# Kernel optimization log

Hardware: AMD Instinct MI355X
Metric: run time of the kernel (lower is better)

Reference implementation:

```python
import jax, jax.numpy as jnp
import numpy as np
import math

V, C, H, L, S, K = 1024, 768, 12, 8, 1024, 10
B, T = 8, 1024
D = C // H


def setup_inputs():
    key = jax.random.key(0)
    ks = jax.random.split(key, 16)
    std = 0.02
    def nrm(k, shape):
        return jax.random.normal(k, shape, jnp.float32) * std
    return {
        "idx": jax.random.randint(ks[0], (B, T), 0, V),
        "y": jax.random.randint(ks[1], (B,), 0, K),
        "tok_emb": nrm(ks[2], (V, C)),
        "pos_emb": nrm(ks[3], (1, S, C)),
        "class_emb": nrm(ks[4], (K, C)),
        "ln1_w": jnp.ones((L, C)), "ln1_b": jnp.zeros((L, C)),
        "attn_w": nrm(ks[5], (L, C, 3 * C)), "attn_b": jnp.zeros((L, 3 * C)),
        "proj_w": nrm(ks[6], (L, C, C)), "proj_b": jnp.zeros((L, C)),
        "ln2_w": jnp.ones((L, C)), "ln2_b": jnp.zeros((L, C)),
        "mlp_w1": nrm(ks[7], (L, C, 4 * C)), "mlp_b1": jnp.zeros((L, 4 * C)),
        "mlp_w2": nrm(ks[8], (L, 4 * C, C)), "mlp_b2": jnp.zeros((L, C)),
        "ln_f_w": jnp.ones((C,)), "ln_f_b": jnp.zeros((C,)),
        "head_w": nrm(ks[9], (C, V)),
    }


def _ln(x, w, b, eps=1e-5):
    m = jnp.mean(x, -1, keepdims=True)
    v = jnp.mean((x - m) ** 2, -1, keepdims=True)
    return (x - m) * jax.lax.rsqrt(v + eps) * w + b


def reference(idx, y, tok_emb, pos_emb, class_emb, ln1_w, ln1_b, attn_w, attn_b,
              proj_w, proj_b, ln2_w, ln2_b, mlp_w1, mlp_b1, mlp_w2, mlp_b2,
              ln_f_w, ln_f_b, head_w):
    Bb, Tt = idx.shape
    # token + positional + class-conditioning embeddings (dropout in eval mode)
    x = tok_emb[idx] + pos_emb[:, :Tt, :] + class_emb[y][:, None, :]
    mask = jnp.tril(jnp.ones((Tt, Tt), bool))
    scale = 1.0 / math.sqrt(D)

    def block(x, p):
        l1w, l1b, aw, ab, pw, pb, l2w, l2b, w1, b1, w2, b2 = p
        h = _ln(x, l1w, l1b)
        qkv = h @ aw + ab                      # [B,T,3C]
        q, k, v = jnp.split(qkv, 3, axis=-1)
        q = q.reshape(Bb, Tt, H, D).transpose(0, 2, 1, 3)
        k = k.reshape(Bb, Tt, H, D).transpose(0, 2, 1, 3)
        v = v.reshape(Bb, Tt, H, D).transpose(0, 2, 1, 3)
        att = jnp.einsum('bhqd,bhkd->bhqk', q, k) * scale
        att = jnp.where(mask, att, -jnp.inf)
        att = jax.nn.softmax(att, axis=-1)
        o = jnp.einsum('bhqk,bhkd->bhqd', att, v)
        o = o.transpose(0, 2, 1, 3).reshape(Bb, Tt, C)
        x = x + o @ pw + pb
        h2 = _ln(x, l2w, l2b)
        x = x + jax.nn.gelu(h2 @ w1 + b1, approximate=False) @ w2 + b2
        return x, None

    x, _ = jax.lax.scan(block, x, (ln1_w, ln1_b, attn_w, attn_b, proj_w, proj_b,
                                   ln2_w, ln2_b, mlp_w1, mlp_b1, mlp_w2, mlp_b2))
    return _ln(x, ln_f_w, ln_f_b) @ head_w
```

## Files before the change

### kernel.cpp

```cpp
#include <hip/hip_runtime.h>
#include <math.h>

#define V_  1024
#define C_  768
#define H_  12
#define L_  8
#define B_  8
#define T_  1024
#define M_  (B_ * T_)
#define C3_ (3 * C_)
#define C4_ (4 * C_)

#define SCL2E 0.18033688011112042592f

typedef __bf16 bf16;
typedef __bf16 bf16x8 __attribute__((ext_vector_type(8)));
typedef float  f32x4  __attribute__((ext_vector_type(4)));
typedef unsigned int u32x4 __attribute__((ext_vector_type(4)));

#define GLDS16(g, l) __builtin_amdgcn_global_load_lds(                       \
    (const __attribute__((address_space(1))) void*)(g),                      \
    (__attribute__((address_space(3))) void*)(l), 16, 0, 0)

__device__ __forceinline__ unsigned short bfb(float f) {
    bf16 h = (bf16)f;
    return __builtin_bit_cast(unsigned short, h);
}

__global__ __launch_bounds__(256) void embed_kernel(
    const int* __restrict__ idx, const int* __restrict__ y,
    const float* __restrict__ tok, const float* __restrict__ pos,
    const float* __restrict__ cls, float* __restrict__ x) {
    int row = blockIdx.x;
    int b = row >> 10, t = row & (T_ - 1);
    int tid = threadIdx.x;
    const float* tr = tok + (size_t)idx[row] * C_;
    const float* pr = pos + (size_t)t * C_;
    const float* cr = cls + (size_t)y[b] * C_;
    float* xr = x + (size_t)row * C_;
    for (int c = tid; c < C_; c += 256)
        xr[c] = tr[c] + pr[c] + cr[c];
}

__device__ __forceinline__ float block_sum256(float v, float* red) {
#pragma unroll
    for (int off = 32; off > 0; off >>= 1) v += __shfl_down(v, off);
    __syncthreads();
    if ((threadIdx.x & 63) == 0) red[threadIdx.x >> 6] = v;
    __syncthreads();
    return red[0] + red[1] + red[2] + red[3];
}

__global__ __launch_bounds__(256) void ln_kernel(
    const float* __restrict__ in, const float* __restrict__ w,
    const float* __restrict__ b, bf16* __restrict__ out) {
    __shared__ float red[4];
    int row = blockIdx.x, tid = threadIdx.x;
    const float* xr = in + (size_t)row * C_;
    float v0 = xr[tid], v1 = xr[tid + 256], v2 = xr[tid + 512];
    float s = block_sum256(v0 + v1 + v2, red);
    float m = s * (1.0f / C_);
    float d0 = v0 - m, d1 = v1 - m, d2 = v2 - m;
    float s2 = block_sum256(d0 * d0 + d1 * d1 + d2 * d2, red);
    float rs = rsqrtf(s2 * (1.0f / C_) + 1e-5f);
    bf16* orow = out + (size_t)row * C_;
    orow[tid]       = (bf16)(d0 * rs * w[tid]       + b[tid]);
    orow[tid + 256] = (bf16)(d1 * rs * w[tid + 256] + b[tid + 256]);
    orow[tid + 512] = (bf16)(d2 * rs * w[tid + 512] + b[tid + 512]);
}

__global__ __launch_bounds__(256) void wt_kernel(
    const float* __restrict__ W, bf16* __restrict__ Wt, int K, int N) {
    __shared__ float ts[32][33];
    const size_t sz = (size_t)K * N;
    const float* Ws = W + blockIdx.z * sz;
    bf16* Wts = Wt + blockIdx.z * sz;
    int n0 = blockIdx.x * 32, k0 = blockIdx.y * 32;
    int tx = threadIdx.x & 31, ty = threadIdx.x >> 5;
#pragma unroll
    for (int i = 0; i < 4; ++i)
        ts[ty + i * 8][tx] = Ws[(size_t)(k0 + ty + i * 8) * N + n0 + tx];
    __syncthreads();
#pragma unroll
    for (int i = 0; i < 4; ++i)
        Wts[(size_t)(n0 + ty + i * 8) * K + k0 + tx] = (bf16)ts[tx][ty + i * 8];
}

template <int ACT, int BIASF, int RESF, int OBF, int VSPLIT>
__global__ __launch_bounds__(256) void mfma_gemm(
    const bf16* __restrict__ A, const bf16* __restrict__ Bt,
    const float* __restrict__ bias, const float* __restrict__ res,
    void* __restrict__ outp, bf16* __restrict__ vt, int K, int N) {
    __shared__ bf16 As[128 * 64];
    __shared__ bf16 Bs[128 * 64];
    const int tid = threadIdx.x;
    const int lane = tid & 63, wave = tid >> 6;
    const int wr = (wave >> 1) * 64, wc = (wave & 1) * 64;
    const int brow = blockIdx.y * 128, bcol = blockIdx.x * 128;
    const int l15 = lane & 15, l4 = lane >> 4;

    const bf16* Ab = A + (size_t)brow * K;
    const bf16* Bb = Bt + (size_t)bcol * K;

    f32x4 acc[4][4];
#pragma unroll
    for (int m = 0; m < 4; ++m)
#pragma unroll
        for (int n = 0; n < 4; ++n)
            acc[m][n] = (f32x4){0.f, 0.f, 0.f, 0.f};

    for (int kt = 0; kt < K; kt += 64) {
        __syncthreads();
#pragma unroll
        for (int i = 0; i < 4; ++i) {
            int j = i * 256 + tid;
            GLDS16(Ab + (size_t)(j >> 3) * K + kt + (j & 7) * 8, As + j * 8);
        }
#pragma unroll
        for (int i = 0; i < 4; ++i) {
            int j = i * 256 + tid;
            GLDS16(Bb + (size_t)(j >> 3) * K + kt + (j & 7) * 8, Bs + j * 8);
        }
        __syncthreads();
#pragma unroll
        for (int kk = 0; kk < 2; ++kk) {
            bf16x8 af[4], bfr[4];
#pragma unroll
            for (int m = 0; m < 4; ++m)
                af[m] = *(const bf16x8*)(As + (wr + m * 16 + l15) * 64 + kk * 32 + l4 * 8);
#pragma unroll
            for (int n = 0; n < 4; ++n)
                bfr[n] = *(const bf16x8*)(Bs + (wc + n * 16 + l15) * 64 + kk * 32 + l4 * 8);
#pragma unroll
            for (int m = 0; m < 4; ++m)
#pragma unroll
                for (int n = 0; n < 4; ++n)
                    acc[m][n] = __builtin_amdgcn_mfma_f32_16x16x32_bf16(
                        af[m], bfr[n], acc[m][n], 0, 0, 0);
        }
    }

    if (VSPLIT && bcol >= 2 * C_) {
#pragma unroll
        for (int n = 0; n < 4; ++n) {
            const int col = bcol + wc + n * 16 + l15;
            const float bv = BIASF ? bias[col] : 0.f;
            const int hh = (col - 2 * C_) >> 6;
            const int dd = (col - 2 * C_) & 63;
#pragma unroll
            for (int m = 0; m < 4; ++m) {
                const int row0 = brow + wr + m * 16 + l4 * 4;
                const int bq = row0 >> 10, t0 = row0 & (T_ - 1);
                ushort4 pk;
                pk.x = bfb(acc[m][n][0] + bv);
                pk.y = bfb(acc[m][n][1] + bv);
                pk.z = bfb(acc[m][n][2] + bv);
                pk.w = bfb(acc[m][n][3] + bv);
                *(ushort4*)&vt[(((size_t)bq * H_ + hh) * 64 + dd) * T_ + t0] = pk;
            }
        }
        return;
    }
#pragma unroll
    for (int n = 0; n < 4; ++n) {
        const int col = bcol + wc + n * 16 + l15;
        const float bv = BIASF ? bias[col] : 0.f;
#pragma unroll
        for (int m = 0; m < 4; ++m) {
#pragma unroll
            for (int j = 0; j < 4; ++j) {
                const int row = brow + wr + m * 16 + l4 * 4 + j;
                float v = acc[m][n][j] + bv;
                if (ACT == 1) v = 0.5f * v * (1.f + erff(v * 0.70710678118654752440f));
                if (VSPLIT && col < C_) v *= SCL2E;
                if (RESF) v += res[(size_t)row * N + col];
                if (OBF)  ((bf16*)outp)[(size_t)row * N + col] = (bf16)v;
                else      ((float*)outp)[(size_t)row * N + col] = v;
            }
        }
    }
}

__device__ __forceinline__ void attn_stage(
    bf16* KN, bf16* VN, int kt,
    const bf16* __restrict__ Kg, const bf16* __restrict__ Vg, int tid) {
    const int r = tid >> 3, bb = tid & 7;
    GLDS16(Kg + (size_t)(kt * 64 + r) * C3_ + ((bb ^ (r & 7)) << 3), KN + tid * 8);
    GLDS16(Vg + (size_t)r * T_ + kt * 64 + ((bb ^ (r & 7)) << 3), VN + tid * 8);
}

__device__ __forceinline__ void attn_step(
    const bf16* KC, const bf16* VC, bf16* KN, bf16* VN,
    const bf16* __restrict__ Kg, const bf16* __restrict__ Vg,
    bf16x8 aq0, bf16x8 aq1, f32x4 (&acc_o)[4], float& mrun, float& lsum,
    int kt, bool pre, bool msk, int qg, int tid, int l15, int g) {
    __syncthreads();
    if (pre) attn_stage(KN, VN, kt + 1, Kg, Vg, tid);
    __builtin_amdgcn_sched_barrier(0);

    f32x4 acc_s[4];
#pragma unroll
    for (int n = 0; n < 4; ++n) acc_s[n] = (f32x4){0.f, 0.f, 0.f, 0.f};
    __builtin_amdgcn_s_setprio(1);
#pragma unroll
    for (int kk = 0; kk < 2; ++kk) {
        bf16x8 aq = kk ? aq1 : aq0;
        const int cb = kk * 64 + g * 16;
#pragma unroll
        for (int n = 0; n < 4; ++n) {
            const int krow = n * 16 + l15;
            bf16x8 bk = *(const bf16x8*)((const char*)KC + krow * 128 +
                                         (cb ^ ((krow & 7) << 4)));
            acc_s[n] = __builtin_amdgcn_mfma_f32_16x16x32_bf16(
                bk, aq, acc_s[n], 0, 0, 0);
        }
    }
    __builtin_amdgcn_s_setprio(0);

    float pv[4][4];
    float rm = -1e30f;
#pragma unroll
    for (int n = 0; n < 4; ++n)
#pragma unroll
        for (int j = 0; j < 4; ++j) {
            float s = acc_s[n][j];
            if (msk && (kt * 64 + n * 16 + g * 4 + j > qg)) s = -1e30f;
            pv[n][j] = s;
            rm = fmaxf(rm, s);
        }
    rm = fmaxf(rm, __shfl_xor(rm, 16));
    rm = fmaxf(rm, __shfl_xor(rm, 32));
    const float mnew = fmaxf(mrun, rm);
    const float fs = exp2f(mrun - mnew);
    mrun = mnew;
    float ps = 0.f;
#pragma unroll
    for (int n = 0; n < 4; ++n)
#pragma unroll
        for (int j = 0; j < 4; ++j) {
            pv[n][j] = exp2f(pv[n][j] - mnew);
            ps += pv[n][j];
        }
    ps += __shfl_xor(ps, 16);
    ps += __shfl_xor(ps, 32);
    lsum = lsum * fs + ps;
#pragma unroll
    for (int n = 0; n < 4; ++n) {
        acc_o[n][0] *= fs; acc_o[n][1] *= fs;
        acc_o[n][2] *= fs; acc_o[n][3] *= fs;
    }

    unsigned int pkw[4][2];
#pragma unroll
    for (int n = 0; n < 4; ++n) {
        pkw[n][0] = ((unsigned int)bfb(pv[n][1]) << 16) | bfb(pv[n][0]);
        pkw[n][1] = ((unsigned int)bfb(pv[n][3]) << 16) | bfb(pv[n][2]);
    }

    const int sA = l15 + (((2 * g) & 3) << 4);
    const int sB = l15 + (((2 * g + 1) & 3) << 4);
    __builtin_amdgcn_s_setprio(1);
#pragma unroll
    for (int kk = 0; kk < 2; ++kk) {
        const unsigned int a0 = __shfl((int)pkw[2 * kk + 0][0], sA);
        const unsigned int a1 = __shfl((int)pkw[2 * kk + 0][1], sA);
        const unsigned int a2 = __shfl((int)pkw[2 * kk + 0][0], sB);
        const unsigned int a3 = __shfl((int)pkw[2 * kk + 0][1], sB);
        const unsigned int b0 = __shfl((int)pkw[2 * kk + 1][0], sA);
        const unsigned int b1 = __shfl((int)pkw[2 * kk + 1][1], sA);
        const unsigned int b2 = __shfl((int)pkw[2 * kk + 1][0], sB);
        const unsigned int b3 = __shfl((int)pkw[2 * kk + 1][1], sB);
        u32x4 wd;
        wd[0] = (g & 2) ? b0 : a0;
        wd[1] = (g & 2) ? b1 : a1;
        wd[2] = (g & 2) ? b2 : a2;
        wd[3] = (g & 2) ? b3 : a3;
        bf16x8 ap = __builtin_bit_cast(bf16x8, wd);
        const int cb = kk * 64 + g * 16;
#pragma unroll
        for (int n = 0; n < 4; ++n) {
            const int drow = n * 16 + l15;
            bf16x8 bv = *(const bf16x8*)((const char*)VC + drow * 128 +
                                         (cb ^ ((drow & 7) << 4)));
            acc_o[n] = __builtin_amdgcn_mfma_f32_16x16x32_bf16(
                bv, ap, acc_o[n], 0, 0, 0);
        }
    }
    __builtin_amdgcn_s_setprio(0);
}

__global__ __launch_bounds__(512, 4) void attn_kernel(
    const bf16* __restrict__ qkv, const bf16* __restrict__ vtb,
    bf16* __restrict__ o) {
    __shared__ bf16 Ks0[64 * 64];
    __shared__ bf16 Vt0[64 * 64];
    __shared__ bf16 Ks1[64 * 64];
    __shared__ bf16 Vt1[64 * 64];

    const int qt = 7 - blockIdx.x;
    const int bh = blockIdx.y;
    const int b = bh / H_, h = bh % H_;
    const int tid = threadIdx.x;
    const int w = tid >> 6, lane = tid & 63;
    const int l15 = lane & 15, g = lane >> 4;
    const int qg = qt * 128 + w * 16 + l15;

    const bf16* Qg = qkv + ((size_t)(b * T_) + qt * 128) * C3_ + h * 64;
    const bf16* Kg = qkv + (size_t)(b * T_) * C3_ + C_ + h * 64;
    const bf16* Vg = vtb + (size_t)bh * 64 * T_;

    bf16x8 aq0 = *(const bf16x8*)(Qg + (size_t)(w * 16 + l15) * C3_ + g * 8);
    bf16x8 aq1 = *(const bf16x8*)(Qg + (size_t)(w * 16 + l15) * C3_ + 32 + g * 8);

    attn_stage(Ks0, Vt0, 0, Kg, Vg, tid);

    f32x4 acc_o[4];
#pragma unroll
    for (int n = 0; n < 4; ++n) acc_o[n] = (f32x4){0.f, 0.f, 0.f, 0.f};
    float mrun = -1e30f, lsum = 0.f;

    const int ktN = 2 * qt + 1;
    const int dmin = 2 * qt + (w >> 2);

    for (int kt = 0; kt < ktN; kt += 2) {
        attn_step(Ks0, Vt0, Ks1, Vt1, Kg, Vg, aq0, aq1, acc_o, mrun, lsum,
                  kt, true, kt >= dmin, qg, tid, l15, g);
        attn_step(Ks1, Vt1, Ks0, Vt0, Kg, Vg, aq0, aq1, acc_o, mrun, lsum,
                  kt + 1, kt + 2 <= ktN, kt + 1 >= dmin, qg, tid, l15, g);
    }

    const float inv = 1.f / lsum;
    bf16* op = o + ((size_t)(b * T_) + qg) * C_ + h * 64;
#pragma unroll
    for (int n = 0; n < 4; ++n) {
        ushort4 pk;
        pk.x = bfb(acc_o[n][0] * inv);
        pk.y = bfb(acc_o[n][1] * inv);
        pk.z = bfb(acc_o[n][2] * inv);
        pk.w = bfb(acc_o[n][3] * inv);
        *(ushort4*)&op[n * 16 + g * 4] = pk;
    }
}

extern "C" void kernel_launch(void* const* d_in, const int* in_sizes, int n_in,
                              void* d_out, int out_size, void* d_ws, size_t ws_size,
                              hipStream_t stream) {
    (void)in_sizes; (void)n_in; (void)out_size; (void)ws_size;
    const int*   idx  = (const int*)d_in[0];
    const int*   y    = (const int*)d_in[1];
    const float* tok  = (const float*)d_in[2];
    const float* pos  = (const float*)d_in[3];
    const float* cls  = (const float*)d_in[4];
    const float* ln1w = (const float*)d_in[5];
    const float* ln1b = (const float*)d_in[6];
    const float* aw   = (const float*)d_in[7];
    const float* ab   = (const float*)d_in[8];
    const float* pw   = (const float*)d_in[9];
    const float* pb   = (const float*)d_in[10];
    const float* ln2w = (const float*)d_in[11];
    const float* ln2b = (const float*)d_in[12];
    const float* w1   = (const float*)d_in[13];
    const float* b1   = (const float*)d_in[14];
    const float* w2   = (const float*)d_in[15];
    const float* b2   = (const float*)d_in[16];
    const float* lnfw = (const float*)d_in[17];
    const float* lnfb = (const float*)d_in[18];
    const float* hw   = (const float*)d_in[19];
    float* out = (float*)d_out;

    char* wsp = (char*)d_ws;
    float* x   = (float*)wsp;  wsp += (size_t)M_ * C_ * 4;
    char*  uni = wsp;          wsp += (size_t)M_ * C4_ * 2;
    bf16*  qkv = (bf16*)uni;
    bf16*  vtb = (bf16*)(uni + (size_t)M_ * C3_ * 2);
    bf16*  mid = (bf16*)uni;
    bf16*  hbf = (bf16*)wsp;   wsp += (size_t)M_ * C_ * 2;
    bf16*  awt = (bf16*)wsp;   wsp += (size_t)L_ * C_ * C3_ * 2;
    bf16*  pwt = (bf16*)wsp;   wsp += (size_t)L_ * C_ * C_  * 2;
    bf16*  w1t = (bf16*)wsp;   wsp += (size_t)L_ * C_ * C4_ * 2;
    bf16*  w2t = (bf16*)wsp;   wsp += (size_t)L_ * C4_ * C_ * 2;
    bf16*  hwt = (bf16*)wsp;   wsp += (size_t)C_ * V_ * 2;

    wt_kernel<<<dim3(C3_ / 32, C_ / 32, L_), 256, 0, stream>>>(aw, awt, C_, C3_);
    wt_kernel<<<dim3(C_ / 32, C_ / 32, L_), 256, 0, stream>>>(pw, pwt, C_, C_);
    wt_kernel<<<dim3(C4_ / 32, C_ / 32, L_), 256, 0, stream>>>(w1, w1t, C_, C4_);
    wt_kernel<<<dim3(C_ / 32, C4_ / 32, L_), 256, 0, stream>>>(w2, w2t, C4_, C_);
    wt_kernel<<<dim3(V_ / 32, C_ / 32, 1), 256, 0, stream>>>(hw, hwt, C_, V_);

    embed_kernel<<<M_, 256, 0, stream>>>(idx, y, tok, pos, cls, x);

    for (int l = 0; l < L_; ++l) {
        ln_kernel<<<M_, 256, 0, stream>>>(x, ln1w + l * C_, ln1b + l * C_, hbf);

        mfma_gemm<0, 1, 0, 1, 1><<<dim3(C3_ / 128, M_ / 128), 256, 0, stream>>>(
            hbf, awt + (size_t)l * C_ * C3_, ab + (size_t)l * C3_, nullptr,
            qkv, vtb, C_, C3_);

        attn_kernel<<<dim3(T_ / 128, B_ * H_), 512, 0, stream>>>(qkv, vtb, hbf);

        mfma_gemm<0, 1, 1, 0, 0><<<dim3(C_ / 128, M_ / 128), 256, 0, stream>>>(
            hbf, pwt + (size_t)l * C_ * C_, pb + (size_t)l * C_, x,
            x, nullptr, C_, C_);

        ln_kernel<<<M_, 256, 0, stream>>>(x, ln2w + l * C_, ln2b + l * C_, hbf);

        mfma_gemm<1, 1, 0, 1, 0><<<dim3(C4_ / 128, M_ / 128), 256, 0, stream>>>(
            hbf, w1t + (size_t)l * C_ * C4_, b1 + (size_t)l * C4_, nullptr,
            mid, nullptr, C_, C4_);

        mfma_gemm<0, 1, 1, 0, 0><<<dim3(C_ / 128, M_ / 128), 256, 0, stream>>>(
            mid, w2t + (size_t)l * C4_ * C_, b2 + (size_t)l * C_, x,
            x, nullptr, C4_, C_);
    }

    ln_kernel<<<M_, 256, 0, stream>>>(x, lnfw, lnfb, hbf);

    mfma_gemm<0, 0, 0, 0, 0><<<dim3(V_ / 128, M_ / 128), 256, 0, stream>>>(
        hbf, hwt, nullptr, nullptr, out, nullptr, C_, V_);
}
```

Before: 2.917 ms.

## Double-buffer GEMM LDS tiles and use one-wave-per-row LayerNorm

The GEMM now holds two LDS buffers and issues the global-to-LDS loads for the next K tile before computing the current one, so memory latency overlaps with MFMA work. LDS use per block doubles to 64KB, which may lower occupancy. Separately, LayerNorm now gives each row to one wave, with float4 loads, a single-pass sum and sum-of-squares reduction through wave shuffles, and packed bf16 stores. This removes the block-level syncs, but the E[x^2]-m^2 variance formula is less numerically robust.

```diff
diff --git a/kernel.cpp b/kernel.cpp
--- a/kernel.cpp
+++ b/kernel.cpp
@@ -42,31 +42,43 @@
         xr[c] = tr[c] + pr[c] + cr[c];
 }
 
-__device__ __forceinline__ float block_sum256(float v, float* red) {
-#pragma unroll
-    for (int off = 32; off > 0; off >>= 1) v += __shfl_down(v, off);
-    __syncthreads();
-    if ((threadIdx.x & 63) == 0) red[threadIdx.x >> 6] = v;
-    __syncthreads();
-    return red[0] + red[1] + red[2] + red[3];
-}
-
 __global__ __launch_bounds__(256) void ln_kernel(
     const float* __restrict__ in, const float* __restrict__ w,
     const float* __restrict__ b, bf16* __restrict__ out) {
-    __shared__ float red[4];
-    int row = blockIdx.x, tid = threadIdx.x;
+    const int row = blockIdx.x * 4 + (threadIdx.x >> 6);
+    const int lane = threadIdx.x & 63;
+    const int c0 = lane * 4;
     const float* xr = in + (size_t)row * C_;
-    float v0 = xr[tid], v1 = xr[tid + 256], v2 = xr[tid + 512];
-    float s = block_sum256(v0 + v1 + v2, red);
-    float m = s * (1.0f / C_);
-    float d0 = v0 - m, d1 = v1 - m, d2 = v2 - m;
-    float s2 = block_sum256(d0 * d0 + d1 * d1 + d2 * d2, red);
-    float rs = rsqrtf(s2 * (1.0f / C_) + 1e-5f);
+    float4 v0 = *(const float4*)&xr[c0];
+    float4 v1 = *(const float4*)&xr[c0 + 256];
+    float4 v2 = *(const float4*)&xr[c0 + 512];
+    float s = v0.x + v0.y + v0.z + v0.w + v1.x + v1.y + v1.z + v1.w +
+              v2.x + v2.y + v2.z + v2.w;
+    float s2 = v0.x * v0.x + v0.y * v0.y + v0.z * v0.z + v0.w * v0.w +
+               v1.x * v1.x + v1.y * v1.y + v1.z * v1.z + v1.w * v1.w +
+               v2.x * v2.x + v2.y * v2.y + v2.z * v2.z + v2.w * v2.w;
+#pragma unroll
+    for (int off = 1; off < 64; off <<= 1) {
+        s  += __shfl_xor(s, off);
+        s2 += __shfl_xor(s2, off);
+    }
+    const float m = s * (1.0f / C_);
+    const float var = s2 * (1.0f / C_) - m * m;
+    const float rs = rsqrtf(var + 1e-5f);
     bf16* orow = out + (size_t)row * C_;
-    orow[tid]       = (bf16)(d0 * rs * w[tid]       + b[tid]);
-    orow[tid + 256] = (bf16)(d1 * rs * w[tid + 256] + b[tid + 256]);
-    orow[tid + 512] = (bf16)(d2 * rs * w[tid + 512] + b[tid + 512]);
+#pragma unroll
+    for (int p = 0; p < 3; ++p) {
+        const int c = c0 + p * 256;
+        float4 v = p == 0 ? v0 : (p == 1 ? v1 : v2);
+        float4 wv = *(const float4*)&w[c];
+        float4 bv = *(const float4*)&b[c];
+        ushort4 pk;
+        pk.x = bfb((v.x - m) * rs * wv.x + bv.x);
+        pk.y = bfb((v.y - m) * rs * wv.y + bv.y);
+        pk.z = bfb((v.z - m) * rs * wv.z + bv.z);
+        pk.w = bfb((v.w - m) * rs * wv.w + bv.w);
+        *(ushort4*)&orow[c] = pk;
+    }
 }
 
 __global__ __launch_bounds__(256) void wt_kernel(
@@ -86,13 +98,51 @@
         Wts[(size_t)(n0 + ty + i * 8) * K + k0 + tx] = (bf16)ts[tx][ty + i * 8];
 }
 
+#define GSTAGE(AS, BS, KT)                                                   \
+    {                                                                        \
+        _Pragma("unroll")                                                    \
+        for (int i = 0; i < 4; ++i) {                                        \
+            int j = i * 256 + tid;                                           \
+            GLDS16(Ab + (size_t)(j >> 3) * K + (KT) + (j & 7) * 8, AS + j * 8); \
+        }                                                                    \
+        _Pragma("unroll")                                                    \
+        for (int i = 0; i < 4; ++i) {                                        \
+            int j = i * 256 + tid;                                           \
+            GLDS16(Bb + (size_t)(j >> 3) * K + (KT) + (j & 7) * 8, BS + j * 8); \
+        }                                                                    \
+    }
+
+#define GCOMP(AS, BS)                                                        \
+    {                                                                        \
+        _Pragma("unroll")                                                    \
+        for (int kk = 0; kk < 2; ++kk) {                                     \
+            bf16x8 af[4], bfr[4];                                            \
+            _Pragma("unroll")                                                \
+            for (int m = 0; m < 4; ++m)                                      \
+                af[m] = *(const bf16x8*)(AS + (wr + m * 16 + l15) * 64 +     \
+                                         kk * 32 + l4 * 8);                  \
+            _Pragma("unroll")                                                \
+            for (int n = 0; n < 4; ++n)                                      \
+                bfr[n] = *(const bf16x8*)(BS + (wc + n * 16 + l15) * 64 +    \
+                                          kk * 32 + l4 * 8);                 \
+            _Pragma("unroll")                                                \
+            for (int m = 0; m < 4; ++m)                                      \
+                _Pragma("unroll")                                            \
+                for (int n = 0; n < 4; ++n)                                  \
+                    acc[m][n] = __builtin_amdgcn_mfma_f32_16x16x32_bf16(     \
+                        af[m], bfr[n], acc[m][n], 0, 0, 0);                  \
+        }                                                                    \
+    }
+
 template <int ACT, int BIASF, int RESF, int OBF, int VSPLIT>
 __global__ __launch_bounds__(256) void mfma_gemm(
     const bf16* __restrict__ A, const bf16* __restrict__ Bt,
     const float* __restrict__ bias, const float* __restrict__ res,
     void* __restrict__ outp, bf16* __restrict__ vt, int K, int N) {
-    __shared__ bf16 As[128 * 64];
-    __shared__ bf16 Bs[128 * 64];
+    __shared__ bf16 As0[128 * 64];
+    __shared__ bf16 Bs0[128 * 64];
+    __shared__ bf16 As1[128 * 64];
+    __shared__ bf16 Bs1[128 * 64];
     const int tid = threadIdx.x;
     const int lane = tid & 63, wave = tid >> 6;
     const int wr = (wave >> 1) * 64, wc = (wave & 1) * 64;
@@ -109,35 +159,17 @@
         for (int n = 0; n < 4; ++n)
             acc[m][n] = (f32x4){0.f, 0.f, 0.f, 0.f};
 
-    for (int kt = 0; kt < K; kt += 64) {
+    GSTAGE(As0, Bs0, 0);
+
+    for (int kt = 0; kt < K; kt += 128) {
         __syncthreads();
-#pragma unroll
-        for (int i = 0; i < 4; ++i) {
-            int j = i * 256 + tid;
-            GLDS16(Ab + (size_t)(j >> 3) * K + kt + (j & 7) * 8, As + j * 8);
-        }
-#pragma unroll
-        for (int i = 0; i < 4; ++i) {
-            int j = i * 256 + tid;
-            GLDS16(Bb + (size_t)(j >> 3) * K + kt + (j & 7) * 8, Bs + j * 8);
-        }
+        if (kt + 64 < K) GSTAGE(As1, Bs1, kt + 64);
+        __builtin_amdgcn_sched_barrier(0);
+        GCOMP(As0, Bs0);
         __syncthreads();
-#pragma unroll
-        for (int kk = 0; kk < 2; ++kk) {
-            bf16x8 af[4], bfr[4];
-#pragma unroll
-            for (int m = 0; m < 4; ++m)
-                af[m] = *(const bf16x8*)(As + (wr + m * 16 + l15) * 64 + kk * 32 + l4 * 8);
-#pragma unroll
-            for (int n = 0; n < 4; ++n)
-                bfr[n] = *(const bf16x8*)(Bs + (wc + n * 16 + l15) * 64 + kk * 32 + l4 * 8);
-#pragma unroll
-            for (int m = 0; m < 4; ++m)
-#pragma unroll
-                for (int n = 0; n < 4; ++n)
-                    acc[m][n] = __builtin_amdgcn_mfma_f32_16x16x32_bf16(
-                        af[m], bfr[n], acc[m][n], 0, 0, 0);
-        }
+        if (kt + 128 < K) GSTAGE(As0, Bs0, kt + 128);
+        __builtin_amdgcn_sched_barrier(0);
+        if (kt + 64 < K) GCOMP(As1, Bs1);
     }
 
     if (VSPLIT && bcol >= 2 * C_) {
@@ -390,7 +422,7 @@
     embed_kernel<<<M_, 256, 0, stream>>>(idx, y, tok, pos, cls, x);
 
     for (int l = 0; l < L_; ++l) {
-        ln_kernel<<<M_, 256, 0, stream>>>(x, ln1w + l * C_, ln1b + l * C_, hbf);
+        ln_kernel<<<M_ / 4, 256, 0, stream>>>(x, ln1w + l * C_, ln1b + l * C_, hbf);
 
         mfma_gemm<0, 1, 0, 1, 1><<<dim3(C3_ / 128, M_ / 128), 256, 0, stream>>>(
             hbf, awt + (size_t)l * C_ * C3_, ab + (size_t)l * C3_, nullptr,
@@ -402,7 +434,7 @@
             hbf, pwt + (size_t)l * C_ * C_, pb + (size_t)l * C_, x,
             x, nullptr, C_, C_);
 
-        ln_kernel<<<M_, 256, 0, stream>>>(x, ln2w + l * C_, ln2b + l * C_, hbf);
+        ln_kernel<<<M_ / 4, 256, 0, stream>>>(x, ln2w + l * C_, ln2b + l * C_, hbf);
 
         mfma_gemm<1, 1, 0, 1, 0><<<dim3(C4_ / 128, M_ / 128), 256, 0, stream>>>(
             hbf, w1t + (size_t)l * C_ * C4_, b1 + (size_t)l * C4_, nullptr,
@@ -413,7 +445,7 @@
             x, nullptr, C4_, C_);
     }
 
-    ln_kernel<<<M_, 256, 0, stream>>>(x, lnfw, lnfb, hbf);
+    ln_kernel<<<M_ / 4, 256, 0, stream>>>(x, lnfw, lnfb, hbf);
 
     mfma_gemm<0, 0, 0, 0, 0><<<dim3(V_ / 128, M_ / 128), 256, 0, stream>>>(
         hbf, hwt, nullptr, nullptr, out, nullptr, C_, V_);
```

Measured after the change: 2.609 ms. 1.12x faster.

## Use 8-wave GEMM tiles and one-wave-per-row layernorm

Applied to the files above, without the earlier changes.

The MFMA GEMM now runs 512 threads per 128x128 tile, with each of 8 waves owning a 64x32 sub-tile instead of 4 waves owning 64x64. This halves accumulator registers per wave and adds more waves to hide load latency, at the cost of more redundant A-fragment LDS reads. LayerNorm now handles one row per wave using float4 loads and shuffle-xor reductions with no shared memory or barriers. It computes variance in a single pass as E[x^2]-m^2, which risks some precision loss.

```diff
diff --git a/kernel.cpp b/kernel.cpp
--- a/kernel.cpp
+++ b/kernel.cpp
@@ -42,31 +42,43 @@
         xr[c] = tr[c] + pr[c] + cr[c];
 }
 
-__device__ __forceinline__ float block_sum256(float v, float* red) {
-#pragma unroll
-    for (int off = 32; off > 0; off >>= 1) v += __shfl_down(v, off);
-    __syncthreads();
-    if ((threadIdx.x & 63) == 0) red[threadIdx.x >> 6] = v;
-    __syncthreads();
-    return red[0] + red[1] + red[2] + red[3];
-}
-
 __global__ __launch_bounds__(256) void ln_kernel(
     const float* __restrict__ in, const float* __restrict__ w,
     const float* __restrict__ b, bf16* __restrict__ out) {
-    __shared__ float red[4];
-    int row = blockIdx.x, tid = threadIdx.x;
+    const int row = blockIdx.x * 4 + (threadIdx.x >> 6);
+    const int lane = threadIdx.x & 63;
+    const int c0 = lane * 4;
     const float* xr = in + (size_t)row * C_;
-    float v0 = xr[tid], v1 = xr[tid + 256], v2 = xr[tid + 512];
-    float s = block_sum256(v0 + v1 + v2, red);
-    float m = s * (1.0f / C_);
-    float d0 = v0 - m, d1 = v1 - m, d2 = v2 - m;
-    float s2 = block_sum256(d0 * d0 + d1 * d1 + d2 * d2, red);
-    float rs = rsqrtf(s2 * (1.0f / C_) + 1e-5f);
+    float4 v0 = *(const float4*)&xr[c0];
+    float4 v1 = *(const float4*)&xr[c0 + 256];
+    float4 v2 = *(const float4*)&xr[c0 + 512];
+    float s = v0.x + v0.y + v0.z + v0.w + v1.x + v1.y + v1.z + v1.w +
+              v2.x + v2.y + v2.z + v2.w;
+    float s2 = v0.x * v0.x + v0.y * v0.y + v0.z * v0.z + v0.w * v0.w +
+               v1.x * v1.x + v1.y * v1.y + v1.z * v1.z + v1.w * v1.w +
+               v2.x * v2.x + v2.y * v2.y + v2.z * v2.z + v2.w * v2.w;
+#pragma unroll
+    for (int off = 1; off < 64; off <<= 1) {
+        s  += __shfl_xor(s, off);
+        s2 += __shfl_xor(s2, off);
+    }
+    const float m = s * (1.0f / C_);
+    const float var = s2 * (1.0f / C_) - m * m;
+    const float rs = rsqrtf(var + 1e-5f);
     bf16* orow = out + (size_t)row * C_;
-    orow[tid]       = (bf16)(d0 * rs * w[tid]       + b[tid]);
-    orow[tid + 256] = (bf16)(d1 * rs * w[tid + 256] + b[tid + 256]);
-    orow[tid + 512] = (bf16)(d2 * rs * w[tid + 512] + b[tid + 512]);
+#pragma unroll
+    for (int p = 0; p < 3; ++p) {
+        const int c = c0 + p * 256;
+        float4 v = p == 0 ? v0 : (p == 1 ? v1 : v2);
+        float4 wv = *(const float4*)&w[c];
+        float4 bv = *(const float4*)&b[c];
+        ushort4 pk;
+        pk.x = bfb((v.x - m) * rs * wv.x + bv.x);
+        pk.y = bfb((v.y - m) * rs * wv.y + bv.y);
+        pk.z = bfb((v.z - m) * rs * wv.z + bv.z);
+        pk.w = bfb((v.w - m) * rs * wv.w + bv.w);
+        *(ushort4*)&orow[c] = pk;
+    }
 }
 
 __global__ __launch_bounds__(256) void wt_kernel(
@@ -87,7 +99,7 @@
 }
 
 template <int ACT, int BIASF, int RESF, int OBF, int VSPLIT>
-__global__ __launch_bounds__(256) void mfma_gemm(
+__global__ __launch_bounds__(512) void mfma_gemm(
     const bf16* __restrict__ A, const bf16* __restrict__ Bt,
     const float* __restrict__ bias, const float* __restrict__ res,
     void* __restrict__ outp, bf16* __restrict__ vt, int K, int N) {
@@ -95,46 +107,47 @@
     __shared__ bf16 Bs[128 * 64];
     const int tid = threadIdx.x;
     const int lane = tid & 63, wave = tid >> 6;
-    const int wr = (wave >> 1) * 64, wc = (wave & 1) * 64;
+    const int wr = (wave >> 2) * 64;
+    const int wc = (wave & 3) * 32;
     const int brow = blockIdx.y * 128, bcol = blockIdx.x * 128;
     const int l15 = lane & 15, l4 = lane >> 4;
 
     const bf16* Ab = A + (size_t)brow * K;
     const bf16* Bb = Bt + (size_t)bcol * K;
 
-    f32x4 acc[4][4];
+    f32x4 acc[4][2];
 #pragma unroll
     for (int m = 0; m < 4; ++m)
 #pragma unroll
-        for (int n = 0; n < 4; ++n)
+        for (int n = 0; n < 2; ++n)
             acc[m][n] = (f32x4){0.f, 0.f, 0.f, 0.f};
 
     for (int kt = 0; kt < K; kt += 64) {
         __syncthreads();
 #pragma unroll
-        for (int i = 0; i < 4; ++i) {
-            int j = i * 256 + tid;
+        for (int i = 0; i < 2; ++i) {
+            int j = i * 512 + tid;
             GLDS16(Ab + (size_t)(j >> 3) * K + kt + (j & 7) * 8, As + j * 8);
         }
 #pragma unroll
-        for (int i = 0; i < 4; ++i) {
-            int j = i * 256 + tid;
+        for (int i = 0; i < 2; ++i) {
+            int j = i * 512 + tid;
             GLDS16(Bb + (size_t)(j >> 3) * K + kt + (j & 7) * 8, Bs + j * 8);
         }
         __syncthreads();
 #pragma unroll
         for (int kk = 0; kk < 2; ++kk) {
-            bf16x8 af[4], bfr[4];
+            bf16x8 af[4], bfr[2];
 #pragma unroll
             for (int m = 0; m < 4; ++m)
                 af[m] = *(const bf16x8*)(As + (wr + m * 16 + l15) * 64 + kk * 32 + l4 * 8);
 #pragma unroll
-            for (int n = 0; n < 4; ++n)
+            for (int n = 0; n < 2; ++n)
                 bfr[n] = *(const bf16x8*)(Bs + (wc + n * 16 + l15) * 64 + kk * 32 + l4 * 8);
 #pragma unroll
             for (int m = 0; m < 4; ++m)
 #pragma unroll
-                for (int n = 0; n < 4; ++n)
+                for (int n = 0; n < 2; ++n)
                     acc[m][n] = __builtin_amdgcn_mfma_f32_16x16x32_bf16(
                         af[m], bfr[n], acc[m][n], 0, 0, 0);
         }
@@ -142,7 +155,7 @@
 
     if (VSPLIT && bcol >= 2 * C_) {
 #pragma unroll
-        for (int n = 0; n < 4; ++n) {
+        for (int n = 0; n < 2; ++n) {
             const int col = bcol + wc + n * 16 + l15;
             const float bv = BIASF ? bias[col] : 0.f;
             const int hh = (col - 2 * C_) >> 6;
@@ -162,7 +175,7 @@
         return;
     }
 #pragma unroll
-    for (int n = 0; n < 4; ++n) {
+    for (int n = 0; n < 2; ++n) {
         const int col = bcol + wc + n * 16 + l15;
         const float bv = BIASF ? bias[col] : 0.f;
 #pragma unroll
@@ -390,31 +403,31 @@
     embed_kernel<<<M_, 256, 0, stream>>>(idx, y, tok, pos, cls, x);
 
     for (int l = 0; l < L_; ++l) {
-        ln_kernel<<<M_, 256, 0, stream>>>(x, ln1w + l * C_, ln1b + l * C_, hbf);
-
-        mfma_gemm<0, 1, 0, 1, 1><<<dim3(C3_ / 128, M_ / 128), 256, 0, stream>>>(
+        ln_kernel<<<M_ / 4, 256, 0, stream>>>(x, ln1w + l * C_, ln1b + l * C_, hbf);
+
+        mfma_gemm<0, 1, 0, 1, 1><<<dim3(C3_ / 128, M_ / 128), 512, 0, stream>>>(
             hbf, awt + (size_t)l * C_ * C3_, ab + (size_t)l * C3_, nullptr,
             qkv, vtb, C_, C3_);
 
         attn_kernel<<<dim3(T_ / 128, B_ * H_), 512, 0, stream>>>(qkv, vtb, hbf);
 
-        mfma_gemm<0, 1, 1, 0, 0><<<dim3(C_ / 128, M_ / 128), 256, 0, stream>>>(
+        mfma_gemm<0, 1, 1, 0, 0><<<dim3(C_ / 128, M_ / 128), 512, 0, stream>>>(
             hbf, pwt + (size_t)l * C_ * C_, pb + (size_t)l * C_, x,
             x, nullptr, C_, C_);
 
-        ln_kernel<<<M_, 256, 0, stream>>>(x, ln2w + l * C_, ln2b + l * C_, hbf);
-
-        mfma_gemm<1, 1, 0, 1, 0><<<dim3(C4_ / 128, M_ / 128), 256, 0, stream>>>(
+        ln_kernel<<<M_ / 4, 256, 0, stream>>>(x, ln2w + l * C_, ln2b + l * C_, hbf);
+
+        mfma_gemm<1, 1, 0, 1, 0><<<dim3(C4_ / 128, M_ / 128), 512, 0, stream>>>(
             hbf, w1t + (size_t)l * C_ * C4_, b1 + (size_t)l * C4_, nullptr,
             mid, nullptr, C_, C4_);
 
-        mfma_gemm<0, 1, 1, 0, 0><<<dim3(C_ / 128, M_ / 128), 256, 0, stream>>>(
+        mfma_gemm<0, 1, 1, 0, 0><<<dim3(C_ / 128, M_ / 128), 512, 0, stream>>>(
             mid, w2t + (size_t)l * C4_ * C_, b2 + (size_t)l * C_, x,
             x, nullptr, C4_, C_);
     }
 
-    ln_kernel<<<M_, 256, 0, stream>>>(x, lnfw, lnfb, hbf);
-
-    mfma_gemm<0, 0, 0, 0, 0><<<dim3(V_ / 128, M_ / 128), 256, 0, stream>>>(
+    ln_kernel<<<M_ / 4, 256, 0, stream>>>(x, lnfw, lnfb, hbf);
+
+    mfma_gemm<0, 0, 0, 0, 0><<<dim3(V_ / 128, M_ / 128), 512, 0, stream>>>(
         hbf, hwt, nullptr, nullptr, out, nullptr, C_, V_);
 }
```

Result: faster. 2.801 ms (-4.0%).
